# Kernel tuning notes

Hardware: AMD Instinct MI355X
Metric: run time of the kernel (lower is better)

## Reference

```python
import jax, jax.numpy as jnp
import numpy as np

DIM = 1024
CTX_DIM = 768
H = 16


def setup_inputs() -> dict:
    key = jax.random.key(0)
    k1, k2, k3, k4, k5 = jax.random.split(key, 5)
    x = jax.random.normal(k1, (2, 2048, DIM), dtype=jnp.float32)
    context = jax.random.normal(k2, (2, 2048, CTX_DIM), dtype=jnp.float32)
    # Linear weights stored as [in, out] (y = x @ W); no biases per module.
    s = 0.02
    Wq = jax.random.normal(k3, (DIM, DIM), dtype=jnp.float32) * s
    Wkv = jax.random.normal(k4, (CTX_DIM, 2 * DIM), dtype=jnp.float32) * s
    Wo = jax.random.normal(k5, (DIM, DIM), dtype=jnp.float32) * s
    return {"x": x, "context": context, "Wq": Wq, "Wkv": Wkv, "Wo": Wo}


def reference(x, context, Wq, Wkv, Wo):
    B, N, C = x.shape
    Dh = C // H  # head dim
    scale = Dh ** -0.5
    M = context.shape[1]
    q = (x @ Wq).reshape(B, N, H, Dh).transpose(0, 2, 1, 3)      # [B,H,N,Dh]
    kv = context @ Wkv                                            # [B,M,2C]
    k, v = jnp.split(kv, 2, axis=-1)
    k = k.reshape(B, M, H, Dh).transpose(0, 2, 1, 3)              # [B,H,M,Dh]
    v = v.reshape(B, M, H, Dh).transpose(0, 2, 1, 3)              # [B,H,M,Dh]
    attn = jax.nn.softmax(jnp.einsum('bhnd,bhmd->bhnm', q, k) * scale, axis=-1)
    out = jnp.einsum('bhnm,bhmd->bhnd', attn, v)                  # [B,H,N,Dh]
    out = out.transpose(0, 2, 1, 3).reshape(B, N, C)
    return out @ Wo  # dropout is identity in eval / p=0
```

## Files before the change

### kernel.cpp

```cpp
#include <hip/hip_runtime.h>

typedef __attribute__((ext_vector_type(4))) float f32x4;
typedef __attribute__((ext_vector_type(8))) short short8;
typedef __attribute__((ext_vector_type(4))) unsigned int u32x4;
typedef __attribute__((ext_vector_type(2))) unsigned int u32x2;
typedef unsigned short u16;
typedef unsigned int u32;

__device__ __forceinline__ u16 f2bf(float f) {
  u32 u = __builtin_bit_cast(u32, f);
  u += 0x7fffu + ((u >> 16) & 1u);
  return (u16)(u >> 16);
}
__device__ __forceinline__ u16 f2bf_t(float f) {
  return (u16)(__builtin_bit_cast(u32, f) >> 16);
}

__device__ __forceinline__ void gl2lds16(const u16* g, const u16* l) {
  __builtin_amdgcn_global_load_lds(
      (const __attribute__((address_space(1))) u32*)g,
      (__attribute__((address_space(3))) u32*)(u32)(unsigned long long)l,
      16, 0, 0);
}

__device__ __forceinline__ void cast_body(const float* __restrict__ s,
                                          u16* __restrict__ d, int blk,
                                          int tid) {
  long i = (long)blk * 256 + tid;
  const f32x4* sp = (const f32x4*)(s + i * 8);
  f32x4 a = sp[0], b = sp[1];
  u16 t[8];
#pragma unroll
  for (int j = 0; j < 4; j++) {
    t[j] = f2bf(a[j]);
    t[4 + j] = f2bf(b[j]);
  }
  *(u32x4*)(d + i * 8) = *(u32x4*)t;
}

__device__ __forceinline__ void transpose_body(const float* __restrict__ W,
                                               u16* __restrict__ WT, int K,
                                               int N, int k0, int n0, int tid,
                                               u16* T) {
#pragma unroll
  for (int i = 0; i < 4; i++) {
    int c = tid + 256 * i;
    int row = c >> 4;
    int ch = c & 15;
    f32x4 f = *(const f32x4*)(W + (long)(k0 + row) * N + n0 + ch * 4);
#pragma unroll
    for (int j = 0; j < 4; j++) T[(ch * 4 + j) * 72 + row] = f2bf(f[j]);
  }
  __syncthreads();
#pragma unroll
  for (int i = 0; i < 2; i++) {
    int c = tid + 256 * i;
    int row = c >> 3;
    int ch = c & 7;
    u32x4 v = *(u32x4*)&T[row * 72 + ch * 8];
    *(u32x4*)(WT + (long)(n0 + row) * K + k0 + ch * 8) = v;
  }
}

__global__ __launch_bounds__(256) void prep(
    const float* __restrict__ x, const float* __restrict__ ctx,
    const float* __restrict__ Wq, const float* __restrict__ Wkv,
    const float* __restrict__ Wo, u16* __restrict__ xb,
    u16* __restrict__ ctxb, u16* __restrict__ wqT, u16* __restrict__ wkvT,
    u16* __restrict__ woT) {
  __shared__ __align__(16) u16 T[64 * 72];
  const int b = blockIdx.x, tid = threadIdx.x;
  if (b < 2048) {
    cast_body(x, xb, b, tid);
  } else if (b < 3584) {
    cast_body(ctx, ctxb, b - 2048, tid);
  } else if (b < 3840) {
    int idx = b - 3584;
    transpose_body(Wq, wqT, 1024, 1024, (idx >> 4) * 64, (idx & 15) * 64, tid, T);
  } else if (b < 4224) {
    int idx = b - 3840;
    transpose_body(Wkv, wkvT, 768, 2048, (idx >> 5) * 64, (idx & 31) * 64, tid, T);
  } else {
    int idx = b - 4224;
    transpose_body(Wo, woT, 1024, 1024, (idx >> 4) * 64, (idx & 15) * 64, tid, T);
  }
}

__device__ __forceinline__ void gemm128_core(
    const u16* __restrict__ A, const u16* __restrict__ Bt, int K, long brow,
    long bcol, int tid, u16* As, u16* Bs, f32x4 (&acc)[4][4]) {
  const int lane = tid & 63, wv = tid >> 6;
  const int l15 = lane & 15, quad = lane >> 4;
  const int wr = (wv >> 1) * 64, wc = (wv & 1) * 64;
  const int sr = lane >> 3, sc = lane & 7;
  const int csw = ((sc ^ sr) & 7) * 8;

  const u16* ag[4];
  const u16* bg[4];
  const u16* al[4];
  const u16* bl[4];
#pragma unroll
  for (int n = 0; n < 4; n++) {
    int row = wv * 32 + n * 8;
    ag[n] = A + (brow + row + sr) * (long)K + csw;
    al[n] = &As[row * 64];
    bg[n] = Bt + (bcol + row + sr) * (long)K + csw;
    bl[n] = &Bs[row * 64];
  }

  for (int kt = 0; kt < K; kt += 64) {
    __syncthreads();
#pragma unroll
    for (int n = 0; n < 4; n++) gl2lds16(ag[n] + kt, al[n]);
#pragma unroll
    for (int n = 0; n < 4; n++) gl2lds16(bg[n] + kt, bl[n]);
    __syncthreads();
#pragma unroll
    for (int kk = 0; kk < 2; kk++) {
      short8 af[4], bf[4];
#pragma unroll
      for (int i = 0; i < 4; i++) {
        int row = wr + i * 16 + l15;
        af[i] = *(short8*)&As[row * 64 + (((kk * 4 + quad) ^ (row & 7)) << 3)];
      }
#pragma unroll
      for (int j = 0; j < 4; j++) {
        int row = wc + j * 16 + l15;
        bf[j] = *(short8*)&Bs[row * 64 + (((kk * 4 + quad) ^ (row & 7)) << 3)];
      }
#pragma unroll
      for (int i = 0; i < 4; i++)
#pragma unroll
        for (int j = 0; j < 4; j++)
          acc[i][j] = __builtin_amdgcn_mfma_f32_16x16x32_bf16(
              af[i], bf[j], acc[i][j], 0, 0, 0);
    }
  }
}

__global__ __launch_bounds__(256, 3) void fused_qkv(
    const u16* __restrict__ xb, const u16* __restrict__ ctxb,
    const u16* __restrict__ wqT, const u16* __restrict__ wkvT,
    u16* __restrict__ Qb, u16* __restrict__ Kb, u16* __restrict__ Vtg,
    float qscale) {
  __shared__ __align__(16) u16 As[128 * 64];
  __shared__ __align__(16) u16 Bs[128 * 64];
  const int tid = threadIdx.x;
  const int lane = tid & 63, wv = tid >> 6;
  const int l15 = lane & 15, quad = lane >> 4;
  const int wr = (wv >> 1) * 64, wc = (wv & 1) * 64;

  f32x4 acc[4][4];
#pragma unroll
  for (int i = 0; i < 4; i++)
#pragma unroll
    for (int j = 0; j < 4; j++) acc[i][j] = (f32x4){0.f, 0.f, 0.f, 0.f};

  int bid = blockIdx.x;
  if (bid < 256) {
    long brow = (long)(bid >> 3) * 128, bcol = (long)(bid & 7) * 128;
    gemm128_core(xb, wqT, 1024, brow, bcol, tid, As, Bs, acc);
#pragma unroll
    for (int i = 0; i < 4; i++)
#pragma unroll
      for (int j = 0; j < 4; j++)
#pragma unroll
        for (int r = 0; r < 4; r++) {
          long row = brow + wr + i * 16 + quad * 4 + r;
          long col = bcol + wc + j * 16 + l15;
          Qb[row * 1024 + col] = f2bf(acc[i][j][r] * qscale);
        }
  } else {
    bid -= 256;
    long brow = (long)(bid >> 4) * 128, bcol = (long)(bid & 15) * 128;
    gemm128_core(ctxb, wkvT, 768, brow, bcol, tid, As, Bs, acc);
    if (bcol < 1024) {
#pragma unroll
      for (int i = 0; i < 4; i++)
#pragma unroll
        for (int j = 0; j < 4; j++)
#pragma unroll
          for (int r = 0; r < 4; r++) {
            long row = brow + wr + i * 16 + quad * 4 + r;
            long col = bcol + wc + j * 16 + l15;
            Kb[row * 1024 + col] = f2bf(acc[i][j][r]);
          }
    } else {
#pragma unroll
      for (int i = 0; i < 4; i++)
#pragma unroll
        for (int j = 0; j < 4; j++) {
          long mg = brow + wr + i * 16 + quad * 4;
          int bb = (int)(mg >> 11);
          int mm = (int)(mg & 2047);
          int tau = mm >> 6, lm = mm & 63;
          int dcol = (int)(bcol + wc + j * 16 + l15) - 1024;
          int h = dcol >> 6, d = dcol & 63;
          int c = ((lm >> 5) & 1) * 4 + ((lm >> 2) & 3);
          int eoff = tau * 64 + (((c ^ (d & 7)) << 3)) + (((lm >> 4) & 1) << 2);
          u32 lo = (u32)f2bf(acc[i][j][0]) | ((u32)f2bf(acc[i][j][1]) << 16);
          u32 hi = (u32)f2bf(acc[i][j][2]) | ((u32)f2bf(acc[i][j][3]) << 16);
          u32x2 v = {lo, hi};
          *(u32x2*)&Vtg[(((long)(bb * 16 + h) * 64 + d) * 2048) + eoff] = v;
        }
    }
  }
}

__global__ __launch_bounds__(256, 3) void gemm_o(
    const u16* __restrict__ A, const u16* __restrict__ Bt,
    float* __restrict__ C) {
  __shared__ __align__(16) u16 As[128 * 64];
  __shared__ __align__(16) u16 Bs[128 * 64];
  const int tid = threadIdx.x;
  const int lane = tid & 63, wv = tid >> 6;
  const int l15 = lane & 15, quad = lane >> 4;
  const int wr = (wv >> 1) * 64, wc = (wv & 1) * 64;
  long brow = (long)blockIdx.y * 128, bcol = (long)blockIdx.x * 128;

  f32x4 acc[4][4];
#pragma unroll
  for (int i = 0; i < 4; i++)
#pragma unroll
    for (int j = 0; j < 4; j++) acc[i][j] = (f32x4){0.f, 0.f, 0.f, 0.f};

  gemm128_core(A, Bt, 1024, brow, bcol, tid, As, Bs, acc);

#pragma unroll
  for (int i = 0; i < 4; i++)
#pragma unroll
    for (int j = 0; j < 4; j++)
#pragma unroll
      for (int r = 0; r < 4; r++) {
        long row = brow + wr + i * 16 + quad * 4 + r;
        long col = bcol + wc + j * 16 + l15;
        C[row * 1024 + col] = acc[i][j][r];
      }
}

__global__ __launch_bounds__(256, 2) void attn_kernel(
    const u16* __restrict__ Q, const u16* __restrict__ Kb,
    const u16* __restrict__ Vtg, u16* __restrict__ AO) {
  __shared__ __align__(16) u16 Vt[64 * 64];
  const int tid = threadIdx.x;
  const int lane = tid & 63, wave = tid >> 6;
  const int l15 = lane & 15, quad = lane >> 4;
  const int bh = blockIdx.y;
  const int b = bh >> 4, h = bh & 15;
  const long qrow0 = (long)b * 2048 + blockIdx.x * 128;

  short8 qf[2][2];
#pragma unroll
  for (int qt = 0; qt < 2; qt++)
#pragma unroll
    for (int kk = 0; kk < 2; kk++)
      qf[qt][kk] = *(const short8*)&Q[(qrow0 + wave * 32 + qt * 16 + l15) * 1024 +
                                      h * 64 + kk * 32 + quad * 8];

  f32x4 O[2][5];
#pragma unroll
  for (int qt = 0; qt < 2; qt++)
#pragma unroll
    for (int dt = 0; dt < 5; dt++) O[qt][dt] = (f32x4){0.f, 0.f, 0.f, 0.f};

  u32x4 ones_u = {0x3F803F80u, 0x3F803F80u, 0x3F803F80u, 0x3F803F80u};
  short8 ones = __builtin_bit_cast(short8, ones_u);

  const u16* kb = Kb + (long)b * 2048 * 1024 + h * 64;
  const u16* vtg = Vtg + (long)(b * 16 + h) * 64 * 2048;
  const u16* vsrc0 = vtg + (long)(wave * 16 + (lane >> 3)) * 2048 + (lane & 7) * 8;
  const u16* vsrc1 = vsrc0 + 8 * 2048;
  const u16* vdst0 = &Vt[(wave * 16) * 64];
  const u16* vdst1 = &Vt[(wave * 16 + 8) * 64];

  for (int mt = 0; mt < 2048; mt += 64) {
    short8 bk[2][4];
#pragma unroll
    for (int kk = 0; kk < 2; kk++)
#pragma unroll
      for (int t = 0; t < 4; t++)
        bk[kk][t] = *(const short8*)&kb[(long)(mt + t * 16 + l15) * 1024 +
                                        kk * 32 + quad * 8];

    __syncthreads();
    gl2lds16(vsrc0 + mt, vdst0);
    gl2lds16(vsrc1 + mt, vdst1);
    __syncthreads();

    f32x4 s[4][2];
#pragma unroll
    for (int m4 = 0; m4 < 4; m4++)
#pragma unroll
      for (int qt = 0; qt < 2; qt++) s[m4][qt] = (f32x4){0.f, 0.f, 0.f, 0.f};
#pragma unroll
    for (int kk = 0; kk < 2; kk++)
#pragma unroll
      for (int m4 = 0; m4 < 4; m4++)
#pragma unroll
        for (int qt = 0; qt < 2; qt++)
          s[m4][qt] = __builtin_amdgcn_mfma_f32_16x16x32_bf16(
              bk[kk][m4], qf[qt][kk], s[m4][qt], 0, 0, 0);

#pragma unroll
    for (int kk = 0; kk < 2; kk++) {
      short8 bv[4];
#pragma unroll
      for (int dt = 0; dt < 4; dt++) {
        int row = dt * 16 + l15;
        bv[dt] = *(short8*)&Vt[row * 64 + (((kk * 4 + quad) ^ (row & 7)) << 3)];
      }
#pragma unroll
      for (int qt = 0; qt < 2; qt++) {
        u32 w[4];
#pragma unroll
        for (int half = 0; half < 2; half++) {
          f32x4 sv = s[2 * kk + half][qt];
          u32 lo = (u32)f2bf_t(__builtin_amdgcn_exp2f(sv[0] - 24.f)) |
                   ((u32)f2bf_t(__builtin_amdgcn_exp2f(sv[1] - 24.f)) << 16);
          u32 hi = (u32)f2bf_t(__builtin_amdgcn_exp2f(sv[2] - 24.f)) |
                   ((u32)f2bf_t(__builtin_amdgcn_exp2f(sv[3] - 24.f)) << 16);
          w[half * 2] = lo;
          w[half * 2 + 1] = hi;
        }
        short8 pa = __builtin_bit_cast(short8, *(u32x4*)w);
#pragma unroll
        for (int dt = 0; dt < 4; dt++)
          O[qt][dt] = __builtin_amdgcn_mfma_f32_16x16x32_bf16(
              pa, bv[dt], O[qt][dt], 0, 0, 0);
        O[qt][4] = __builtin_amdgcn_mfma_f32_16x16x32_bf16(
            pa, ones, O[qt][4], 0, 0, 0);
      }
    }
  }

#pragma unroll
  for (int qt = 0; qt < 2; qt++) {
    float inv[4];
#pragma unroll
    for (int r = 0; r < 4; r++) inv[r] = 1.f / O[qt][4][r];
#pragma unroll
    for (int dt = 0; dt < 4; dt++)
#pragma unroll
      for (int r = 0; r < 4; r++) {
        long row = qrow0 + wave * 32 + qt * 16 + quad * 4 + r;
        int col = h * 64 + dt * 16 + l15;
        AO[row * 1024 + col] = f2bf(O[qt][dt][r] * inv[r]);
      }
  }
}

extern "C" void kernel_launch(void* const* d_in, const int* in_sizes, int n_in,
                              void* d_out, int out_size, void* d_ws,
                              size_t ws_size, hipStream_t stream) {
  const float* x = (const float*)d_in[0];
  const float* ctx = (const float*)d_in[1];
  const float* Wq = (const float*)d_in[2];
  const float* Wkv = (const float*)d_in[3];
  const float* Wo = (const float*)d_in[4];
  float* out = (float*)d_out;

  u16* ws = (u16*)d_ws;
  u16* wqT = ws;
  u16* wkvT = wqT + 1048576;
  u16* woT = wkvT + 1572864;
  u16* Qb = woT + 1048576;
  u16* Kb = Qb + 4194304;
  u16* Vtg = Kb + 4194304;
  u16* xb = Vtg + 4194304;
  u16* ctxb = xb + 4194304;
  u16* AOb = xb;

  const float qscale = 0.125f * 1.4426950408889634f;

  prep<<<dim3(4480), 256, 0, stream>>>(x, ctx, Wq, Wkv, Wo, xb, ctxb, wqT,
                                       wkvT, woT);

  fused_qkv<<<dim3(768), 256, 0, stream>>>(xb, ctxb, wqT, wkvT, Qb, Kb, Vtg,
                                           qscale);

  attn_kernel<<<dim3(16, 32), 256, 0, stream>>>(Qb, Kb, Vtg, AOb);

  gemm_o<<<dim3(8, 32), 256, 0, stream>>>(AOb, woT, out);
}
```

Measured before the change: 203.8 us.

## Prefetch K in registers, load V directly, and split-K the output GEMM

The attention kernel no longer stages V through shared memory with two block barriers per tile. Each wave now reads V fragments directly from global memory and double-buffers the K fragments so the next tile's loads overlap the current MFMAs. The output projection GEMM is split into two K halves across a third grid dimension and accumulates with float atomics into an output zeroed by a memset. This removes barriers and doubles the output GEMM's parallelism, at the cost of more global/L2 traffic for V, more registers, atomic traffic and an extra memset.

Result: slower. 248.7 us (+22.1%).

```diff
diff --git a/kernel.cpp b/kernel.cpp
--- a/kernel.cpp
+++ b/kernel.cpp
@@ -87,8 +87,9 @@
 }
 
 __device__ __forceinline__ void gemm128_core(
-    const u16* __restrict__ A, const u16* __restrict__ Bt, int K, long brow,
-    long bcol, int tid, u16* As, u16* Bs, f32x4 (&acc)[4][4]) {
+    const u16* __restrict__ A, const u16* __restrict__ Bt, int Kstride,
+    int Klen, long brow, long bcol, int tid, u16* As, u16* Bs,
+    f32x4 (&acc)[4][4]) {
   const int lane = tid & 63, wv = tid >> 6;
   const int l15 = lane & 15, quad = lane >> 4;
   const int wr = (wv >> 1) * 64, wc = (wv & 1) * 64;
@@ -102,13 +103,13 @@
 #pragma unroll
   for (int n = 0; n < 4; n++) {
     int row = wv * 32 + n * 8;
-    ag[n] = A + (brow + row + sr) * (long)K + csw;
+    ag[n] = A + (brow + row + sr) * (long)Kstride + csw;
     al[n] = &As[row * 64];
-    bg[n] = Bt + (bcol + row + sr) * (long)K + csw;
+    bg[n] = Bt + (bcol + row + sr) * (long)Kstride + csw;
     bl[n] = &Bs[row * 64];
   }
 
-  for (int kt = 0; kt < K; kt += 64) {
+  for (int kt = 0; kt < Klen; kt += 64) {
     __syncthreads();
 #pragma unroll
     for (int n = 0; n < 4; n++) gl2lds16(ag[n] + kt, al[n]);
@@ -159,7 +160,7 @@
   int bid = blockIdx.x;
   if (bid < 256) {
     long brow = (long)(bid >> 3) * 128, bcol = (long)(bid & 7) * 128;
-    gemm128_core(xb, wqT, 1024, brow, bcol, tid, As, Bs, acc);
+    gemm128_core(xb, wqT, 1024, 1024, brow, bcol, tid, As, Bs, acc);
 #pragma unroll
     for (int i = 0; i < 4; i++)
 #pragma unroll
@@ -173,7 +174,7 @@
   } else {
     bid -= 256;
     long brow = (long)(bid >> 4) * 128, bcol = (long)(bid & 15) * 128;
-    gemm128_core(ctxb, wkvT, 768, brow, bcol, tid, As, Bs, acc);
+    gemm128_core(ctxb, wkvT, 768, 768, brow, bcol, tid, As, Bs, acc);
     if (bcol < 1024) {
 #pragma unroll
       for (int i = 0; i < 4; i++)
@@ -217,6 +218,7 @@
   const int l15 = lane & 15, quad = lane >> 4;
   const int wr = (wv >> 1) * 64, wc = (wv & 1) * 64;
   long brow = (long)blockIdx.y * 128, bcol = (long)blockIdx.x * 128;
+  int k0 = blockIdx.z * 512;
 
   f32x4 acc[4][4];
 #pragma unroll
@@ -224,7 +226,7 @@
 #pragma unroll
     for (int j = 0; j < 4; j++) acc[i][j] = (f32x4){0.f, 0.f, 0.f, 0.f};
 
-  gemm128_core(A, Bt, 1024, brow, bcol, tid, As, Bs, acc);
+  gemm128_core(A + k0, Bt + k0, 1024, 512, brow, bcol, tid, As, Bs, acc);
 
 #pragma unroll
   for (int i = 0; i < 4; i++)
@@ -234,14 +236,13 @@
       for (int r = 0; r < 4; r++) {
         long row = brow + wr + i * 16 + quad * 4 + r;
         long col = bcol + wc + j * 16 + l15;
-        C[row * 1024 + col] = acc[i][j][r];
+        atomicAdd(&C[row * 1024 + col], acc[i][j][r]);
       }
 }
 
 __global__ __launch_bounds__(256, 2) void attn_kernel(
-    const u16* __restrict__ Q, const u16* __restrict__ Kb,
+    const u16* __restrict__ Q, const u16* __restrict__ Kg,
     const u16* __restrict__ Vtg, u16* __restrict__ AO) {
-  __shared__ __align__(16) u16 Vt[64 * 64];
   const int tid = threadIdx.x;
   const int lane = tid & 63, wave = tid >> 6;
   const int l15 = lane & 15, quad = lane >> 4;
@@ -266,26 +267,35 @@
   u32x4 ones_u = {0x3F803F80u, 0x3F803F80u, 0x3F803F80u, 0x3F803F80u};
   short8 ones = __builtin_bit_cast(short8, ones_u);
 
-  const u16* kb = Kb + (long)b * 2048 * 1024 + h * 64;
+  const u16* kb = Kg + (long)b * 2048 * 1024 + h * 64;
   const u16* vtg = Vtg + (long)(b * 16 + h) * 64 * 2048;
-  const u16* vsrc0 = vtg + (long)(wave * 16 + (lane >> 3)) * 2048 + (lane & 7) * 8;
-  const u16* vsrc1 = vsrc0 + 8 * 2048;
-  const u16* vdst0 = &Vt[(wave * 16) * 64];
-  const u16* vdst1 = &Vt[(wave * 16 + 8) * 64];
-
-  for (int mt = 0; mt < 2048; mt += 64) {
-    short8 bk[2][4];
+  const u16* kfb[2][4];
+  const u16* vfb[2][4];
+#pragma unroll
+  for (int kk = 0; kk < 2; kk++)
+#pragma unroll
+    for (int t = 0; t < 4; t++) {
+      int row = t * 16 + l15;
+      kfb[kk][t] = kb + (long)row * 1024 + kk * 32 + quad * 8;
+      vfb[kk][t] = vtg + (long)row * 2048 + (((kk * 4 + quad) ^ (row & 7)) << 3);
+    }
+
+  auto load_k = [&](short8(&kf)[2][4], int mt) {
 #pragma unroll
     for (int kk = 0; kk < 2; kk++)
 #pragma unroll
       for (int t = 0; t < 4; t++)
-        bk[kk][t] = *(const short8*)&kb[(long)(mt + t * 16 + l15) * 1024 +
-                                        kk * 32 + quad * 8];
-
-    __syncthreads();
-    gl2lds16(vsrc0 + mt, vdst0);
-    gl2lds16(vsrc1 + mt, vdst1);
-    __syncthreads();
+        kf[kk][t] = *(const short8*)(kfb[kk][t] + (long)mt * 1024);
+  };
+
+  auto step = [&](short8(&kc)[2][4], short8(&kn)[2][4], int mt) {
+    short8 vf[2][4];
+#pragma unroll
+    for (int kk = 0; kk < 2; kk++)
+#pragma unroll
+      for (int dt = 0; dt < 4; dt++)
+        vf[kk][dt] = *(const short8*)(vfb[kk][dt] + mt);
+    if (mt + 64 < 2048) load_k(kn, mt + 64);
 
     f32x4 s[4][2];
 #pragma unroll
@@ -299,16 +309,10 @@
 #pragma unroll
         for (int qt = 0; qt < 2; qt++)
           s[m4][qt] = __builtin_amdgcn_mfma_f32_16x16x32_bf16(
-              bk[kk][m4], qf[qt][kk], s[m4][qt], 0, 0, 0);
+              kc[kk][m4], qf[qt][kk], s[m4][qt], 0, 0, 0);
 
 #pragma unroll
     for (int kk = 0; kk < 2; kk++) {
-      short8 bv[4];
-#pragma unroll
-      for (int dt = 0; dt < 4; dt++) {
-        int row = dt * 16 + l15;
-        bv[dt] = *(short8*)&Vt[row * 64 + (((kk * 4 + quad) ^ (row & 7)) << 3)];
-      }
 #pragma unroll
       for (int qt = 0; qt < 2; qt++) {
         u32 w[4];
@@ -326,11 +330,18 @@
 #pragma unroll
         for (int dt = 0; dt < 4; dt++)
           O[qt][dt] = __builtin_amdgcn_mfma_f32_16x16x32_bf16(
-              pa, bv[dt], O[qt][dt], 0, 0, 0);
+              pa, vf[kk][dt], O[qt][dt], 0, 0, 0);
         O[qt][4] = __builtin_amdgcn_mfma_f32_16x16x32_bf16(
             pa, ones, O[qt][4], 0, 0, 0);
       }
     }
+  };
+
+  short8 ka[2][4], kbuf[2][4];
+  load_k(ka, 0);
+  for (int mt = 0; mt < 2048; mt += 128) {
+    step(ka, kbuf, mt);
+    step(kbuf, ka, mt + 64);
   }
 
 #pragma unroll
@@ -372,6 +383,8 @@
 
   const float qscale = 0.125f * 1.4426950408889634f;
 
+  hipMemsetAsync(out, 0, (size_t)4096 * 1024 * sizeof(float), stream);
+
   prep<<<dim3(4480), 256, 0, stream>>>(x, ctx, Wq, Wkv, Wo, xb, ctxb, wqT,
                                        wkvT, woT);
 
@@ -380,5 +393,5 @@
 
   attn_kernel<<<dim3(16, 32), 256, 0, stream>>>(Qb, Kb, Vtg, AOb);
 
-  gemm_o<<<dim3(8, 32), 256, 0, stream>>>(AOb, woT, out);
-}
+  gemm_o<<<dim3(8, 32, 2), 256, 0, stream>>>(AOb, woT, out);
+}
```
